# Kernel tuning notes

Hardware: AMD Instinct MI355X
Metric: run time of the kernel (lower is better)

The kernel has to match this reference:

```python
import jax, jax.numpy as jnp
import numpy as np

D_MODEL = 1024; D_STATE = 128; HEADDIM = 64; D_CONV = 4; CHUNK = 256
D_INNER = 2 * D_MODEL; NHEADS = D_INNER // HEADDIM
CONV_DIM = D_INNER + 2 * D_STATE
D_IN_PROJ = 2 * D_INNER + 2 * D_STATE + NHEADS
POOL_SIZE = 50; SUMMARY_DIM = 64; TAU1 = 0.5; TAU2 = 0.3
RET_HEAD_DIM = SUMMARY_DIM // 4  # CrossTokenRetrieval n_heads=4
SCORER_HID = int(D_MODEL * 0.25)
B_SZ = 2; T_LEN = 1024
EPS = 1e-5


def _rmsnorm(x, w):
    var = jnp.mean(jnp.square(x), axis=-1, keepdims=True)
    return x * jax.lax.rsqrt(var + EPS) * w


def _ssd(xd, dA, Bm, Cm):
    # Mamba2 SSD chunked scan. xd=(b,T,h,p)=x*dt, dA=(b,T,h)=dt*A, Bm/Cm=(b,T,n)
    b, T, h, p = xd.shape
    c = T // CHUNK; l = CHUNK
    xd = xd.reshape(b, c, l, h, p)
    dA = dA.reshape(b, c, l, h).transpose(0, 3, 1, 2)           # (b,h,c,l)
    Bm = Bm.reshape(b, c, l, -1); Cm = Cm.reshape(b, c, l, -1)  # (b,c,l,n)
    cs = jnp.cumsum(dA, axis=-1)                                # (b,h,c,l)
    mask = jnp.tril(jnp.ones((l, l), bool))
    seg = jnp.where(mask, cs[..., :, None] - cs[..., None, :], -jnp.inf)
    L = jnp.exp(seg)                                            # (b,h,c,l,s)
    y_diag = jnp.einsum('bcln,bcsn,bhcls,bcshp->bclhp', Cm, Bm, L, xd)
    decay_states = jnp.exp(cs[..., -1:] - cs)                   # (b,h,c,l)
    states = jnp.einsum('bcln,bhcl,bclhp->bchpn', Bm, decay_states, xd)
    chunk_sum = jnp.pad(cs[..., -1], ((0, 0), (0, 0), (1, 0)))  # (b,h,c+1)
    cs2 = jnp.cumsum(chunk_sum, axis=-1)
    maskc = jnp.tril(jnp.ones((c + 1, c + 1), bool))
    segc = jnp.where(maskc, cs2[..., :, None] - cs2[..., None, :], -jnp.inf)
    decay_chunk = jnp.exp(segc)                                 # (b,h,c+1,c+1)
    states = jnp.concatenate([jnp.zeros_like(states[:, :1]), states], axis=1)
    prev = jnp.einsum('bhzc,bchpn->bzhpn', decay_chunk, states)[:, :-1]
    y_off = jnp.einsum('bcln,bchpn,bhcl->bclhp', Cm, prev, jnp.exp(cs))
    return (y_diag + y_off).reshape(b, T, h, p)


def _forward(x, norm_w, in_proj_w, conv_w, conv_b, dt_bias, A_log, D, ssm_norm_w,
             out_proj_w, scorer_w1, scorer_w2, summ_w, q_w, k_w, v_w, gate_w):
    b, T, _ = x.shape
    residual = x
    xn = _rmsnorm(x, norm_w)
    # --- Mamba2 ---
    zxbcdt = xn @ in_proj_w                                     # (b,T,4384)
    z = zxbcdt[..., :D_INNER]
    xBC = zxbcdt[..., D_INNER:D_INNER + CONV_DIM]
    dt = jax.nn.softplus(zxbcdt[..., -NHEADS:] + dt_bias)       # (b,T,h)
    xpad = jnp.pad(xBC, ((0, 0), (D_CONV - 1, 0), (0, 0)))      # causal depthwise conv
    conv = conv_b + sum(xpad[:, k:k + T, :] * conv_w[:, k] for k in range(D_CONV))
    xBC = jax.nn.silu(conv)
    xs = xBC[..., :D_INNER].reshape(b, T, NHEADS, HEADDIM)
    Bm = xBC[..., D_INNER:D_INNER + D_STATE]
    Cm = xBC[..., D_INNER + D_STATE:]
    A = -jnp.exp(A_log)                                         # (h,)
    y = _ssd(xs * dt[..., None], dt * A, Bm, Cm)
    y = y + xs * D[None, None, :, None]
    y = y.reshape(b, T, D_INNER)
    y = _rmsnorm(y * jax.nn.silu(z), ssm_norm_w)                # gated RMSNorm
    y = y @ out_proj_w                                          # (b,T,d_model)
    # --- token importance scorer ---
    scores = jax.nn.sigmoid(jax.nn.relu(y @ scorer_w1) @ scorer_w2)[..., 0]  # (b,T)
    # --- memory pool update (layer_idx % freq == 0) ---
    summaries = (y @ summ_w).reshape(-1, SUMMARY_DIM)
    flat_scores = scores.reshape(-1)

    def step(carry, inp):
        pool, prios, count = carry
        s, sc = inp
        valid = sc > TAU1
        not_full = count < POOL_SIZE
        min_idx = jnp.argmin(prios)
        idx = jnp.where(not_full, count, min_idx)
        write = valid & (not_full | (sc > prios[min_idx]))
        pool = pool.at[idx].set(jnp.where(write, s, pool[idx]))
        prios = prios.at[idx].set(jnp.where(write, sc, prios[idx]))
        count = count + (valid & not_full).astype(jnp.int32)
        return (pool, prios, count), None

    init = (jnp.zeros((POOL_SIZE, SUMMARY_DIM), y.dtype),
            jnp.zeros((POOL_SIZE,), y.dtype), jnp.int32(0))
    (pool, prios, count), _ = jax.lax.scan(step, init, (summaries, flat_scores))
    # --- retrieval + gated fusion ---
    q = y @ q_w                                                 # (b,T,S)
    kk = pool @ k_w                                             # (P,S)
    vv = pool @ v_w                                             # (P,d_model)
    logits = jnp.einsum('bts,ps->btp', q, kk) / (RET_HEAD_DIM ** 0.5)
    valid_slot = jnp.arange(POOL_SIZE) < count
    logits = jnp.where(valid_slot, logits, -1e9)
    retrieved = jnp.einsum('btp,pd->btd', jax.nn.softmax(logits, axis=-1), vv)
    gate = jax.nn.sigmoid(jnp.concatenate([y, retrieved], axis=-1) @ gate_w)
    cond = (jnp.mean(scores) > TAU2) & (count > 0)
    y = jnp.where(cond, y + gate * retrieved, y)
    return residual + y


def setup_inputs() -> dict:
    key = jax.random.key(0)
    ks = jax.random.split(key, 16)
    w = lambda k, shape, s=0.02: jax.random.normal(k, shape, jnp.float32) * s
    dt = jax.random.uniform(ks[5], (NHEADS,), jnp.float32, 0.001, 0.1)
    return {
        'x': jax.random.normal(ks[0], (B_SZ, T_LEN, D_MODEL), jnp.float32),
        'norm_w': jnp.ones((D_MODEL,), jnp.float32),
        'in_proj_w': w(ks[1], (D_MODEL, D_IN_PROJ)),
        'conv_w': w(ks[2], (CONV_DIM, D_CONV), 0.1),
        'conv_b': jnp.zeros((CONV_DIM,), jnp.float32),
        'dt_bias': jnp.log(jnp.expm1(dt)),
        'A_log': jnp.log(jax.random.uniform(ks[6], (NHEADS,), jnp.float32, 1.0, 16.0)),
        'D': jnp.ones((NHEADS,), jnp.float32),
        'ssm_norm_w': jnp.ones((D_INNER,), jnp.float32),
        'out_proj_w': w(ks[7], (D_INNER, D_MODEL)),
        'scorer_w1': w(ks[8], (D_MODEL, SCORER_HID)),
        'scorer_w2': w(ks[9], (SCORER_HID, 1), 0.2),
        'summ_w': w(ks[10], (D_MODEL, SUMMARY_DIM)),
        'q_w': w(ks[11], (D_MODEL, SUMMARY_DIM)),
        'k_w': w(ks[12], (SUMMARY_DIM, SUMMARY_DIM)),
        'v_w': w(ks[13], (SUMMARY_DIM, D_MODEL)),
        'gate_w': w(ks[14], (2 * D_MODEL, D_MODEL)),
    }


def reference(x, norm_w, in_proj_w, conv_w, conv_b, dt_bias, A_log, D, ssm_norm_w,
              out_proj_w, scorer_w1, scorer_w2, summ_w, q_w, k_w, v_w, gate_w):
    return _forward(x, norm_w, in_proj_w, conv_w, conv_b, dt_bias, A_log, D, ssm_norm_w,
                    out_proj_w, scorer_w1, scorer_w2, summ_w, q_w, k_w, v_w, gate_w)
```

## Files before the change

### kernel.cpp

```cpp
#include <hip/hip_runtime.h>
#include <math.h>

#define NHEADS 32
#define D_INNER 2048
#define CONV_DIM 2304
#define D_IN_PROJ 4384
#define POOL_N 50
#define BT 2048

typedef __attribute__((ext_vector_type(8))) short short8;
typedef __attribute__((ext_vector_type(4))) float f32x4;

__device__ __forceinline__ float sigmoidf_(float x){ return 1.f/(1.f+expf(-x)); }
__device__ __forceinline__ ushort f2bf(float f){
  union{float f; unsigned u;} v; v.f=f;
  unsigned r = v.u + 0x7fffu + ((v.u>>16)&1u);
  return (ushort)(r>>16);
}
__device__ __forceinline__ void gload16(const void* g, void* l){
  __builtin_amdgcn_global_load_lds(
    (const __attribute__((address_space(1))) unsigned int*)g,
    (__attribute__((address_space(3))) unsigned int*)l, 16, 0, 0);
}

__global__ __launch_bounds__(256) void k_rmsnorm_x(const float* __restrict__ x, const float* __restrict__ w, ushort* __restrict__ xn){
  int r = blockIdx.x;
  const float* xr = x + (size_t)r*1024;
  float v[4]; float ss=0.f;
  for(int i=0;i<4;i++){ v[i]=xr[threadIdx.x+i*256]; ss+=v[i]*v[i]; }
  __shared__ float red[4];
  for(int off=32;off;off>>=1) ss += __shfl_down(ss,off,64);
  int wid=threadIdx.x>>6, lane=threadIdx.x&63;
  if(lane==0) red[wid]=ss;
  __syncthreads();
  float tot=red[0]+red[1]+red[2]+red[3];
  float rs=rsqrtf(tot*(1.f/1024.f)+1e-5f);
  for(int i=0;i<4;i++){ int c=threadIdx.x+i*256; xn[(size_t)r*1024+c]=f2bf(v[i]*rs*w[c]); }
}

__global__ __launch_bounds__(256) void k_transpose_cvt(const float* __restrict__ src, ushort* __restrict__ dst, int R, int C){
  __shared__ float tile[32][33];
  int c0 = blockIdx.x*32, r0 = blockIdx.y*32;
  int tx = threadIdx.x&31, ty = threadIdx.x>>5;
  for(int i=0;i<4;i++){ int r = r0+ty+i*8; tile[ty+i*8][tx] = src[(size_t)r*C + c0+tx]; }
  __syncthreads();
  for(int i=0;i<4;i++){ int c = c0+ty+i*8; dst[(size_t)c*R + r0+tx] = f2bf(tile[tx][ty+i*8]); }
}

__global__ __launch_bounds__(256) void gemm_bf16(const ushort* __restrict__ A, const ushort* __restrict__ Bt,
    float* __restrict__ C, ushort* __restrict__ Cb, int M, int N, int K, int act, int nbx){
  __shared__ __align__(16) ushort As[128*32];
  __shared__ __align__(16) ushort Bs[128*32];
  int wg = blockIdx.x, nwg = gridDim.x;
  if((nwg & 7)==0){ int cpx = nwg>>3; wg = (wg&7)*cpx + (wg>>3); }
  int bx = wg % nbx, by = wg / nbx;
  int n0 = bx*128, m0 = by*128;
  int tid = threadIdx.x;
  int lane = tid&63, w = tid>>6;
  int wr = (w>>1)*64, wc = (w&1)*64;
  f32x4 acc[4][4];
  for(int i=0;i<4;i++)for(int j=0;j<4;j++)acc[i][j]=(f32x4){0.f,0.f,0.f,0.f};
  int srow0 = w*32 + (lane>>2);
  int sbyte = (lane&3)*16;
  const char* AG0 = (const char*)(A + (size_t)(m0+srow0)*K) + sbyte;
  const char* AG1 = (const char*)(A + (size_t)(m0+srow0+16)*K) + sbyte;
  int brow0 = n0+srow0, brow1 = n0+srow0+16;
  bool bv0 = brow0 < N, bv1 = brow1 < N;
  const char* BG0 = (const char*)(Bt + (size_t)(bv0?brow0:0)*K) + sbyte;
  const char* BG1 = (const char*)(Bt + (size_t)(bv1?brow1:0)*K) + sbyte;
  char* Al0 = (char*)As + w*2048; char* Al1 = Al0 + 1024;
  char* Bl0 = (char*)Bs + w*2048; char* Bl1 = Bl0 + 1024;
  int fr = lane&15, fko = (lane>>4)*8;
  for(int k0=0;k0<K;k0+=32){
    gload16(AG0 + (size_t)k0*2, Al0);
    gload16(AG1 + (size_t)k0*2, Al1);
    if(bv0) gload16(BG0 + (size_t)k0*2, Bl0);
    if(bv1) gload16(BG1 + (size_t)k0*2, Bl1);
    __syncthreads();
    short8 af[4], bfr[4];
    for(int i=0;i<4;i++) af[i]  = *(const short8*)(As + (wr+i*16+fr)*32 + fko);
    for(int j=0;j<4;j++) bfr[j] = *(const short8*)(Bs + (wc+j*16+fr)*32 + fko);
    for(int i=0;i<4;i++)
      for(int j=0;j<4;j++)
        acc[i][j] = __builtin_amdgcn_mfma_f32_16x16x32_bf16(af[i], bfr[j], acc[i][j], 0,0,0);
    __syncthreads();
  }
  int rbase = m0 + wr + (lane>>4)*4;
  for(int i=0;i<4;i++){
    for(int j=0;j<4;j++){
      int col = n0 + wc + j*16 + fr;
      if(col < N){
        for(int r=0;r<4;r++){
          float v = acc[i][j][r];
          if(act) v = fmaxf(v,0.f);
          size_t idx = (size_t)(rbase + i*16 + r)*N + col;
          C[idx] = v;
          if(Cb) Cb[idx] = f2bf(v);
        }
      }
    }
  }
}

__global__ void k_dt(const float* __restrict__ zxb, const float* __restrict__ dt_bias, float* __restrict__ dtb){
  int o = blockIdx.x*256+threadIdx.x;
  int r = o>>5, h = o&31;
  float v = zxb[(size_t)r*D_IN_PROJ + 4352 + h] + dt_bias[h];
  dtb[o] = (v>20.f) ? v : log1pf(expf(v));
}

__global__ void k_conv4(const float* __restrict__ zxb, const float* __restrict__ cw, const float* __restrict__ cb, float* __restrict__ xbc){
  int o = blockIdx.x*256+threadIdx.x;
  if(o >= 2048*576) return;
  int ch4 = (o % 576)*4; int rt = o / 576;
  int b = rt>>10, t = rt&1023;
  float a[4];
  { float4 cbv = *(const float4*)(cb + ch4); a[0]=cbv.x; a[1]=cbv.y; a[2]=cbv.z; a[3]=cbv.w; }
  float cwa[4][4];
  for(int c2=0;c2<4;c2++){
    float4 v = *(const float4*)(cw + (ch4+c2)*4);
    cwa[c2][0]=v.x; cwa[c2][1]=v.y; cwa[c2][2]=v.z; cwa[c2][3]=v.w;
  }
  for(int k=0;k<4;k++){
    int tt = t-3+k;
    if(tt>=0){
      float4 v = *(const float4*)(zxb + (size_t)(b*1024+tt)*D_IN_PROJ + 2048 + ch4);
      a[0] += v.x*cwa[0][k]; a[1] += v.y*cwa[1][k];
      a[2] += v.z*cwa[2][k]; a[3] += v.w*cwa[3][k];
    }
  }
  float4 o4;
  o4.x = a[0]*sigmoidf_(a[0]); o4.y = a[1]*sigmoidf_(a[1]);
  o4.z = a[2]*sigmoidf_(a[2]); o4.w = a[3]*sigmoidf_(a[3]);
  *(float4*)(xbc + (size_t)rt*CONV_DIM + ch4) = o4;
}

__global__ __launch_bounds__(256) void k_gt(const float* __restrict__ xbc, float* __restrict__ Gt){
  int bc = blockIdx.x >> 8;
  int tile = blockIdx.x & 255;
  int l0 = (tile>>4)<<4, s0 = (tile&15)<<4;
  int b = bc>>2, c = bc&3;
  int row0 = b*1024 + c*256;
  __shared__ float Cs[16][130], Bs2[16][130];
  int tid = threadIdx.x;
  for(int i=0;i<8;i++){ int e=tid+i*256; int rr=e>>7, n=e&127;
    Cs[rr][n]  = xbc[(size_t)(row0+l0+rr)*CONV_DIM + 2176 + n];
    Bs2[rr][n] = xbc[(size_t)(row0+s0+rr)*CONV_DIM + 2048 + n];
  }
  __syncthreads();
  int tx = tid&15, ty = tid>>4;
  float acc=0.f;
  for(int n=0;n<128;n++) acc += Cs[tx][n]*Bs2[ty][n];
  Gt[(size_t)bc*65536 + (size_t)(s0+ty)*256 + (l0+tx)] = acc;
}

__global__ __launch_bounds__(512) void k_ssd1w(const float* __restrict__ xbc, const float* __restrict__ dtb,
    const float* __restrict__ A_log, const float* __restrict__ Gt,
    float* __restrict__ ybuf, float* __restrict__ states, float* __restrict__ csb, float* __restrict__ sdA){
  int blk = blockIdx.x;
  int bc = blk>>5, h = blk&31;
  int b = bc>>2, c = bc&3;
  int row0 = b*1024 + c*256;
  int tid = threadIdx.x;
  __shared__ float cs[256];
  __shared__ float dts[256];
  __shared__ float dec[256];
  __shared__ __align__(16) ushort xdT[64*256];
  __shared__ __align__(16) ushort Mw[4*64*32];
  __shared__ __align__(16) ushort Bw[4*32*256];
  float Ah = -expf(A_log[h]);
  if(tid < 256){
    float dtv = dtb[(size_t)(row0+tid)*32 + h];
    dts[tid] = dtv;
    cs[tid] = dtv*Ah;
  }
  __syncthreads();
  for(int o=1;o<256;o<<=1){
    float add = 0.f;
    if(tid<256 && tid>=o) add = cs[tid-o];
    __syncthreads();
    if(tid<256) cs[tid] += add;
    __syncthreads();
  }
  float cslast = cs[255];
  if(tid < 256){
    float csl = cs[tid];
    csb[blk*256+tid] = csl;
    dec[tid] = expf(cslast - csl);
    if(tid==0) sdA[blk] = cslast;
  }
  {
    int p = tid&63, g = tid>>6;
    for(int i=0;i<32;i++){
      int l = g + 8*i;
      float v = xbc[(size_t)(row0+l)*CONV_DIM + h*64 + p] * dts[l];
      int off = ((p<<9) + (l<<1)) ^ ((p&7)<<4);
      *(ushort*)((char*)xdT + off) = f2bf(v);
    }
  }
  __syncthreads();

  int w = tid>>6, lane = tid&63;
  int fr = lane&15, fq = lane>>4;
  const float* gt = Gt + (size_t)bc*65536;
  if(w < 4){
    int rowl = w*64 + lane;
    float csl_w = cs[rowl];
    f32x4 accY[4][4];
    for(int i=0;i<4;i++)for(int j=0;j<4;j++)accY[i][j]=(f32x4){0.f,0.f,0.f,0.f};
    int nk = 2*(w+1);
    for(int ks=0; ks<nk; ks++){
      int s0 = ks*32;
      float cs_s0 = cs[s0];
      float ev = expf(cs_s0 - cs[s0 + (lane&31)]);
      float el = expf(csl_w - cs_s0);
      for(int j=0;j<4;j++){
        short8 mp;
        for(int k=0;k<8;k++){
          int s2 = j*8+k;
          int s = s0 + s2;
          float gv = gt[(size_t)s*256 + rowl];
          float esv = __shfl(ev, s2, 64);
          float m = (s <= rowl) ? gv*el*esv : 0.f;
          mp[k] = (short)f2bf(m);
        }
        int off = (w<<12) + ((((lane)<<6) + (j<<4)) ^ ((lane&7)<<4));
        *(short8*)((char*)Mw + off) = mp;
      }
      asm volatile("s_waitcnt lgkmcnt(0)" ::: "memory");
      __builtin_amdgcn_sched_barrier(0);
      short8 af[4], bv4[4];
      for(int i=0;i<4;i++){
        int lp = i*16 + fr;
        int off = (w<<12) + (((lp<<6) + (fq<<4)) ^ ((lp&7)<<4));
        af[i] = *(const short8*)((char*)Mw + off);
      }
      for(int j=0;j<4;j++){
        int p = j*16 + fr;
        int off = ((p<<9) + ((s0 + fq*8)<<1)) ^ ((p&7)<<4);
        bv4[j] = *(const short8*)((char*)xdT + off);
      }
      for(int i=0;i<4;i++)
        for(int j=0;j<4;j++)
          accY[i][j] = __builtin_amdgcn_mfma_f32_16x16x32_bf16(af[i], bv4[j], accY[i][j], 0,0,0);
      asm volatile("" ::: "memory");
    }
    for(int i=0;i<4;i++){
      int l = 64*w + i*16 + fq*4;
      for(int j=0;j<4;j++){
        int p = j*16 + fr;
        for(int r=0;r<4;r++)
          ybuf[(size_t)(row0+l+r)*2048 + h*64 + p] = accY[i][j][r];
      }
    }
  } else {
    int sw = w-4, nbase = sw*32;
    {
      int nn = lane&31, half = lane>>5;
      for(int i=0;i<128;i++){
        int l = half + 2*i;
        float v = xbc[(size_t)(row0+l)*CONV_DIM + 2048 + nbase + nn] * dec[l];
        int off = (sw<<14) + (((nn<<9) + (l<<1)) ^ ((nn&7)<<4));
        *(ushort*)((char*)Bw + off) = f2bf(v);
      }
    }
    asm volatile("s_waitcnt lgkmcnt(0)" ::: "memory");
    __builtin_amdgcn_sched_barrier(0);
    f32x4 accS[4][2];
    for(int i=0;i<4;i++)for(int j=0;j<2;j++)accS[i][j]=(f32x4){0.f,0.f,0.f,0.f};
    for(int ks=0;ks<8;ks++){
      int l0 = ks*32;
      short8 aS[4], bS[2];
      for(int i=0;i<4;i++){
        int p = i*16 + fr;
        int off = ((p<<9) + ((l0+fq*8)<<1)) ^ ((p&7)<<4);
        aS[i] = *(const short8*)((char*)xdT + off);
      }
      for(int j=0;j<2;j++){
        int nn = j*16 + fr;
        int off = (sw<<14) + (((nn<<9) + ((l0+fq*8)<<1)) ^ ((nn&7)<<4));
        bS[j] = *(const short8*)((char*)Bw + off);
      }
      for(int i=0;i<4;i++)
        for(int j=0;j<2;j++)
          accS[i][j] = __builtin_amdgcn_mfma_f32_16x16x32_bf16(aS[i], bS[j], accS[i][j], 0,0,0);
    }
    for(int i=0;i<4;i++){
      int p = i*16 + fq*4;
      for(int j=0;j<2;j++){
        int n = nbase + j*16 + fr;
        for(int r=0;r<4;r++)
          states[(size_t)blk*8192 + (size_t)(p+r)*128 + n] = accS[i][j][r];
      }
    }
  }
}

__global__ __launch_bounds__(256) void k_ssd2(const float* __restrict__ states, const float* __restrict__ sdA, float* __restrict__ prevb){
  int idx = blockIdx.x*256 + threadIdx.x;
  int e = idx & 8191;
  int h = (idx >> 13) & 31;
  int b = idx >> 18;
  float run = 0.f;
  for(int c=0;c<4;c++){
    int sblk = (b*4+c)*32 + h;
    size_t base = (size_t)sblk*8192 + e;
    prevb[base] = run;
    run = (run + states[base]) * expf(sdA[sblk]);
  }
}

__global__ __launch_bounds__(256) void k_ssd3m(const float* __restrict__ xbc, const float* __restrict__ csb,
    const float* __restrict__ prevb, const float* __restrict__ Dp, float* __restrict__ ybuf){
  int blk = blockIdx.x; int bc = blk>>5, h = blk&31; int b=bc>>2, c=bc&3;
  int row0 = b*1024+c*256;
  int tid = threadIdx.x;
  __shared__ __align__(16) ushort Cs[256*128];
  __shared__ __align__(16) ushort Ps[64*128];
  __shared__ float cse[256];
  for(int i=0;i<128;i++){
    int id = tid + i*256;
    int n = id & 127, l = id >> 7;
    float v = xbc[(size_t)(row0+l)*CONV_DIM + 2176 + n];
    int off = ((l<<8) + (n<<1)) ^ ((l&7)<<4);
    *(ushort*)((char*)Cs + off) = f2bf(v);
  }
  for(int i=0;i<32;i++){
    int id = tid + i*256;
    int n = id & 127, p = id >> 7;
    float v = prevb[(size_t)blk*8192 + id];
    int off = ((p<<8) + (n<<1)) ^ ((p&7)<<4);
    *(ushort*)((char*)Ps + off) = f2bf(v);
  }
  cse[tid] = expf(csb[blk*256+tid]);
  __syncthreads();
  int w=tid>>6, lane=tid&63, fr=lane&15, fq=lane>>4;
  f32x4 acc[4][4];
  for(int i=0;i<4;i++)for(int j=0;j<4;j++)acc[i][j]=(f32x4){0.f,0.f,0.f,0.f};
  for(int ks=0;ks<4;ks++){
    int n0 = ks*32;
    short8 af[4], bf_[4];
    for(int i=0;i<4;i++){
      int l = w*64 + i*16 + fr;
      int off = ((l<<8) + ((n0+fq*8)<<1)) ^ ((l&7)<<4);
      af[i] = *(const short8*)((char*)Cs + off);
    }
    for(int j=0;j<4;j++){
      int p = j*16 + fr;
      int off = ((p<<8) + ((n0+fq*8)<<1)) ^ ((p&7)<<4);
      bf_[j] = *(const short8*)((char*)Ps + off);
    }
    for(int i=0;i<4;i++)
      for(int j=0;j<4;j++)
        acc[i][j] = __builtin_amdgcn_mfma_f32_16x16x32_bf16(af[i], bf_[j], acc[i][j], 0,0,0);
  }
  float Dh = Dp[h];
  for(int i=0;i<4;i++){
    int lbase = 64*w + i*16 + fq*4;
    for(int r=0;r<4;r++){
      int l = lbase + r;
      float e = cse[l];
      size_t rowoff = (size_t)(row0+l)*CONV_DIM + h*64;
      size_t yb = (size_t)(row0+l)*2048 + h*64;
      for(int j=0;j<4;j++){
        int p = j*16 + fr;
        float xs = xbc[rowoff + p];
        ybuf[yb+p] += e*acc[i][j][r] + xs*Dh;
      }
    }
  }
}

__global__ __launch_bounds__(256) void k_gate_norm(const float* __restrict__ y, const float* __restrict__ zxb,
    const float* __restrict__ w, ushort* __restrict__ yb16){
  int r = blockIdx.x;
  const float* zr = zxb + (size_t)r*D_IN_PROJ;
  const float* yr = y + (size_t)r*2048;
  float v[8]; float ss=0.f;
  for(int i=0;i<8;i++){ int c=threadIdx.x+i*256; float z=zr[c]; float g=yr[c]*(z*sigmoidf_(z)); v[i]=g; ss+=g*g; }
  __shared__ float red[4];
  for(int off=32;off;off>>=1) ss += __shfl_down(ss,off,64);
  int wid=threadIdx.x>>6, lane=threadIdx.x&63;
  if(lane==0) red[wid]=ss;
  __syncthreads();
  float tot=red[0]+red[1]+red[2]+red[3];
  float rs=rsqrtf(tot*(1.f/2048.f)+1e-5f);
  for(int i=0;i<8;i++){ int c=threadIdx.x+i*256; yb16[(size_t)r*2048+c]=f2bf(v[i]*rs*w[c]); }
}

__global__ void k_scorer2(const float* __restrict__ h1, const float* __restrict__ w2, float* __restrict__ scores){
  int r = blockIdx.x; int lane = threadIdx.x;
  float s=0.f;
  for(int k=0;k<4;k++){ int c=lane+k*64; s += h1[(size_t)r*256+c]*w2[c]; }
  for(int off=32;off;off>>=1) s += __shfl_down(s,off,64);
  if(lane==0) scores[r]=sigmoidf_(s);
}

__global__ void k_pool(const float* __restrict__ scores,
                       int* __restrict__ countws, int* __restrict__ winners, float* __restrict__ condf){
  __shared__ float scs[BT];
  int lane = threadIdx.x;
  float own[32];
  float ssum = 0.f; int vcnt = 0;
  #pragma unroll
  for(int i=0;i<32;i++){
    float s0 = scores[i*64 + lane];
    own[i] = s0; scs[i*64+lane] = s0;
    ssum += s0; vcnt += (s0 > 0.5f) ? 1 : 0;
  }
  float ts = ssum; int tv = vcnt;
  for(int off=32;off;off>>=1){ ts += __shfl_xor(ts,off,64); tv += __shfl_xor(tv,off,64); }
  int count = tv < POOL_N ? tv : POOL_N;
  bool fallback = false;
  if(tv <= POOL_N){
    int base = 0;
    #pragma unroll
    for(int i=0;i<32;i++){
      bool sel = own[i] > 0.5f;
      unsigned long long mask = __ballot(sel);
      int pre = __popcll(mask & ((1ull<<lane)-1ull));
      if(sel) winners[base + pre] = i*64 + lane;
      base += __popcll(mask);
    }
    for(int r=base+lane; r<POOL_N; r+=64) winners[r] = -1;
  } else {
    unsigned lo = 0u, hi = 0x3F800000u;
    while(hi - lo > 1u){
      unsigned mid = (lo + hi) >> 1;
      float midf = __uint_as_float(mid);
      int cnt = 0;
      #pragma unroll
      for(int i=0;i<32;i++) cnt += (own[i] >= midf) ? 1 : 0;
      for(int off=32;off;off>>=1) cnt += __shfl_xor(cnt,off,64);
      if(cnt >= POOL_N) lo = mid; else hi = mid;
    }
    float v50 = __uint_as_float(lo);
    int cl = 0;
    #pragma unroll
    for(int i=0;i<32;i++) cl += (own[i] >= v50) ? 1 : 0;
    for(int off=32;off;off>>=1) cl += __shfl_xor(cl,off,64);
    if(cl == POOL_N){
      int base = 0;
      #pragma unroll
      for(int i=0;i<32;i++){
        bool sel = own[i] >= v50;
        unsigned long long mask = __ballot(sel);
        int pre = __popcll(mask & ((1ull<<lane)-1ull));
        if(sel) winners[base + pre] = i*64 + lane;
        base += __popcll(mask);
      }
    } else fallback = true;
  }
  if(fallback){
    float prio = 0.f; int winner = -1; int cnt2 = 0;
    float curmin = 0.f; int curargmin = 0;
    for(int b0=0;b0<BT;b0+=64){
      float ow = scs[b0+lane];
      unsigned long long mask = (cnt2 < POOL_N) ? __ballot(ow > 0.5f) : __ballot(ow > curmin);
      while(mask){
        int j = __ffsll(mask) - 1;
        mask &= mask - 1ull;
        float sc = __shfl(ow, j, 64);
        if(cnt2 < POOL_N){
          if(lane == cnt2){ prio = sc; winner = b0+j; }
          cnt2++;
          if(cnt2 == POOL_N){
            float v = (lane < POOL_N)? prio : INFINITY; int idx = lane;
            for(int off=32;off;off>>=1){
              float ov = __shfl_xor(v,off,64); int oi = __shfl_xor(idx,off,64);
              if(ov < v || (ov==v && oi<idx)){ v=ov; idx=oi; }
            }
            curmin = v; curargmin = idx;
          }
        } else if(sc > curmin){
          if(lane == curargmin){ prio = sc; winner = b0+j; }
          float v = (lane < POOL_N)? prio : INFINITY; int idx = lane;
          for(int off=32;off;off>>=1){
            float ov = __shfl_xor(v,off,64); int oi = __shfl_xor(idx,off,64);
            if(ov < v || (ov==v && oi<idx)){ v=ov; idx=oi; }
          }
          curmin = v; curargmin = idx;
        }
      }
    }
    if(lane < POOL_N) winners[lane] = winner;
  }
  if(lane==0){
    countws[0] = count;
    float mean = ts*(1.f/2048.f);
    condf[0] = (mean>0.3f && count>0)? 1.f : 0.f;
  }
}

__global__ void k_poolg(const float* __restrict__ sq, const int* __restrict__ winners, float* __restrict__ poolb){
  int p = blockIdx.x; int lane = threadIdx.x;
  int wi = winners[p];
  poolb[p*64+lane] = (wi>=0)? sq[(size_t)wi*128+lane] : 0.f;
}

__global__ void k_kk(const float* __restrict__ pool, const float* __restrict__ k_w, float* __restrict__ kkT){
  int o = blockIdx.x*256+threadIdx.x;
  if(o >= 64*POOL_N) return;
  int j = o/POOL_N, p = o%POOL_N;
  float s=0.f;
  for(int k=0;k<64;k++) s += pool[p*64+k]*k_w[k*64+j];
  kkT[j*64+p]=s;
}

__global__ void k_vvT(const float* __restrict__ pool, const float* __restrict__ v_w, ushort* __restrict__ vvT){
  int o = blockIdx.x*256+threadIdx.x;
  if(o >= 1024*64) return;
  int d = o>>6, p = o&63;
  float s=0.f;
  if(p < POOL_N)
    for(int k=0;k<64;k++) s += pool[p*64+k]*v_w[(size_t)k*1024+d];
  vvT[o] = f2bf(s);
}

__global__ __launch_bounds__(256) void k_probs(const float* __restrict__ sq, const float* __restrict__ kkT,
    const int* __restrict__ counti, ushort* __restrict__ Pb){
  __shared__ float qs[4][64];
  int tid = threadIdx.x;
  int w = tid>>6, lane = tid&63;
  int r = blockIdx.x*4 + w;
  qs[w][lane] = sq[(size_t)r*128 + 64 + lane];
  __syncthreads();
  int count = counti[0];
  float logit = -1e9f;
  if(lane < POOL_N && lane < count){
    float s=0.f;
    for(int k=0;k<64;k++) s += qs[w][k]*kkT[k*64+lane];
    logit = s*0.25f;
  }
  float m = logit;
  for(int off=32;off;off>>=1) m = fmaxf(m, __shfl_xor(m,off,64));
  float e = expf(logit-m);
  float sum = e;
  for(int off=32;off;off>>=1) sum += __shfl_xor(sum,off,64);
  Pb[(size_t)r*64 + lane] = f2bf(e/sum);
}

__global__ __launch_bounds__(256) void k_pv(const ushort* __restrict__ Pb, const ushort* __restrict__ vvT,
    float* __restrict__ retr){
  __shared__ __align__(16) ushort As[128*64];
  __shared__ __align__(16) ushort Bs[128*64];
  int m0 = (blockIdx.x >> 3)*128, n0 = (blockIdx.x & 7)*128;
  int tid = threadIdx.x;
  int row = tid>>1, half = tid&1;
  {
    const uint4* sa = (const uint4*)(Pb  + (size_t)(m0+row)*64 + half*32);
    const uint4* sb = (const uint4*)(vvT + (size_t)(n0+row)*64 + half*32);
    for(int ch=0;ch<4;ch++){
      int boff = (row<<7) + (half<<6) + (ch<<4);
      int so = boff ^ ((row&7)<<4);
      *(uint4*)((char*)As + so) = sa[ch];
      *(uint4*)((char*)Bs + so) = sb[ch];
    }
  }
  __syncthreads();
  int w=tid>>6, lane=tid&63, fr=lane&15, fq=lane>>4;
  int wr=(w>>1)*64, wc=(w&1)*64;
  f32x4 acc[4][4];
  for(int i=0;i<4;i++)for(int j=0;j<4;j++)acc[i][j]=(f32x4){0.f,0.f,0.f,0.f};
  for(int k0=0;k0<64;k0+=32){
    short8 af[4], bf_[4];
    for(int i=0;i<4;i++){
      int r = wr+i*16+fr;
      int boff = ((r<<7) + ((k0+fq*8)<<1)) ^ ((r&7)<<4);
      af[i] = *(const short8*)((char*)As + boff);
    }
    for(int j=0;j<4;j++){
      int r = wc+j*16+fr;
      int boff = ((r<<7) + ((k0+fq*8)<<1)) ^ ((r&7)<<4);
      bf_[j] = *(const short8*)((char*)Bs + boff);
    }
    for(int i=0;i<4;i++)
      for(int j=0;j<4;j++)
        acc[i][j] = __builtin_amdgcn_mfma_f32_16x16x32_bf16(af[i], bf_[j], acc[i][j], 0,0,0);
  }
  int rbase = m0 + wr + fq*4;
  for(int i=0;i<4;i++){
    for(int j=0;j<4;j++){
      int col = n0 + wc + j*16 + fr;
      for(int r=0;r<4;r++)
        retr[(size_t)(rbase + i*16 + r)*1024 + col] = acc[i][j][r];
    }
  }
}

__global__ void k_concat(const float* __restrict__ yout, const float* __restrict__ retr, ushort* __restrict__ cc){
  int o = blockIdx.x*256+threadIdx.x;
  int r = o>>11, c2 = o&2047;
  cc[o] = f2bf((c2<1024)? yout[(size_t)r*1024+c2] : retr[(size_t)r*1024+(c2-1024)]);
}

__global__ void k_final(const float* __restrict__ x, const float* __restrict__ yout, const float* __restrict__ g,
   const float* __restrict__ retr, const float* __restrict__ condf, float* __restrict__ out){
  int o = blockIdx.x*256+threadIdx.x;
  float gv = sigmoidf_(g[o]);
  out[o] = x[o] + yout[o] + condf[0]*gv*retr[o];
}

static inline void gemmb(hipStream_t s, const ushort*A,const ushort*Bt,float*C,ushort*Cb,int M,int N,int K,int act){
  int nbx = (N+127)/128;
  int nwg = nbx * (M/128);
  hipLaunchKernelGGL(gemm_bf16,dim3(nwg),dim3(256),0,s,A,Bt,C,Cb,M,N,K,act,nbx);
}

extern "C" void kernel_launch(void* const* d_in, const int* in_sizes, int n_in,
                              void* d_out, int out_size, void* d_ws, size_t ws_size,
                              hipStream_t stream) {
  const float* x        = (const float*)d_in[0];
  const float* norm_w   = (const float*)d_in[1];
  const float* in_proj_w= (const float*)d_in[2];
  const float* conv_w   = (const float*)d_in[3];
  const float* conv_b   = (const float*)d_in[4];
  const float* dt_bias  = (const float*)d_in[5];
  const float* A_log    = (const float*)d_in[6];
  const float* Dp       = (const float*)d_in[7];
  const float* ssm_norm_w=(const float*)d_in[8];
  const float* out_proj_w=(const float*)d_in[9];
  const float* scorer_w1= (const float*)d_in[10];
  const float* scorer_w2= (const float*)d_in[11];
  const float* summ_w   = (const float*)d_in[12];
  const float* q_w      = (const float*)d_in[13];
  const float* k_w      = (const float*)d_in[14];
  const float* v_w      = (const float*)d_in[15];
  const float* gate_w   = (const float*)d_in[16];
  float* out = (float*)d_out;

  unsigned char* base = (unsigned char*)d_ws;
  size_t off = 0;
  auto FB = [&](size_t bytes)->void*{ void* p = base+off; off = (off+bytes+255)&~(size_t)255; return p; };
  float* zxb   = (float*)FB((size_t)2048*D_IN_PROJ*4);
  float* dtb   = (float*)FB((size_t)2048*32*4);
  float* xbc   = (float*)FB((size_t)2048*CONV_DIM*4);
  float* csb   = (float*)FB((size_t)256*256*4);
  float* sdA   = (float*)FB(1024);
  float* states= (float*)FB((size_t)256*8192*4);
  float* prevb = (float*)FB((size_t)256*8192*4);
  float* ybuf  = (float*)FB((size_t)2048*2048*4);
  float* yout  = (float*)FB((size_t)2048*1024*4);
  float* scores= (float*)FB(2048*4);
  float* summ  = (float*)FB((size_t)2048*64*4);
  float* qb    = (float*)FB((size_t)2048*64*4);
  float* poolb = (float*)FB(POOL_N*64*4);
  float* prios = (float*)FB(256);
  float* miscf = (float*)FB(256);
  int*   counti= (int*)FB(256);
  int*   winners=(int*)FB(256);
  unsigned char* RX = (unsigned char*)FB((size_t)4194304);
  unsigned char* W1 = (unsigned char*)FB((size_t)8978432);

  ushort* xnb   = (ushort*)RX;
  ushort* sqT   = (ushort*)RX;
  ushort* summT = (ushort*)RX;
  ushort* qT    = (ushort*)(RX + 131072);
  float*  h1    = (float*) (RX + 262144);
  float*  kkT   = (float*) (RX + 2359296);
  ushort* vvT   = (ushort*)(RX + 2375680);
  ushort* Pb    = (ushort*)(RX + 2506752);
  ushort* inT   = (ushort*)W1;
  ushort* outT  = (ushort*)W1;
  ushort* gateT = (ushort*)(W1 + 4194304);
  ushort* sc1T  = (ushort*)(W1 + 8388608);
  float*  Gt    = yout;
  ushort* ybf   = (ushort*)prevb;
  float*  gbuf  = prevb;
  float*  retr  = states;
  ushort* ccb   = (ushort*)ybuf;
  ushort* youtb = (ushort*)((unsigned char*)ybuf + 8388608);
  float*  sq    = summ;
  (void)qb; (void)prios;

  hipLaunchKernelGGL(k_transpose_cvt, dim3(137,32), dim3(256), 0, stream, in_proj_w, inT, 1024, 4384);
  k_rmsnorm_x<<<2048,256,0,stream>>>(x, norm_w, xnb);
  gemmb(stream, xnb, inT, zxb, nullptr, 2048, D_IN_PROJ, 1024, 0);
  hipLaunchKernelGGL(k_transpose_cvt, dim3(32,64), dim3(256), 0, stream, out_proj_w, outT, 2048, 1024);
  hipLaunchKernelGGL(k_transpose_cvt, dim3(32,64), dim3(256), 0, stream, gate_w, gateT, 2048, 1024);
  hipLaunchKernelGGL(k_transpose_cvt, dim3(8,32), dim3(256), 0, stream, scorer_w1, sc1T, 1024, 256);
  hipLaunchKernelGGL(k_transpose_cvt, dim3(2,32), dim3(256), 0, stream, summ_w, summT, 1024, 64);
  hipLaunchKernelGGL(k_transpose_cvt, dim3(2,32), dim3(256), 0, stream, q_w, qT, 1024, 64);
  k_dt<<<256,256,0,stream>>>(zxb, dt_bias, dtb);
  k_conv4<<<4608,256,0,stream>>>(zxb, conv_w, conv_b, xbc);
  k_gt<<<2048,256,0,stream>>>(xbc, Gt);
  k_ssd1w<<<256,512,0,stream>>>(xbc, dtb, A_log, Gt, ybuf, states, csb, sdA);
  k_ssd2<<<2048,256,0,stream>>>(states, sdA, prevb);
  k_ssd3m<<<256,256,0,stream>>>(xbc, csb, prevb, Dp, ybuf);
  k_gate_norm<<<2048,256,0,stream>>>(ybuf, zxb, ssm_norm_w, ybf);
  gemmb(stream, ybf, outT, yout, youtb, 2048, 1024, 2048, 0);
  gemmb(stream, youtb, sc1T, h1, nullptr, 2048, 256, 1024, 1);
  k_scorer2<<<2048,64,0,stream>>>(h1, scorer_w2, scores);
  gemmb(stream, youtb, sqT, sq, nullptr, 2048, 128, 1024, 0);
  k_pool<<<1,64,0,stream>>>(scores, counti, winners, miscf);
  k_poolg<<<POOL_N,64,0,stream>>>(sq, winners, poolb);
  k_kk<<<(64*POOL_N+255)/256,256,0,stream>>>(poolb, k_w, kkT);
  k_vvT<<<256,256,0,stream>>>(poolb, v_w, vvT);
  k_probs<<<512,256,0,stream>>>(sq, kkT, counti, Pb);
  k_pv<<<128,256,0,stream>>>(Pb, vvT, retr);
  k_concat<<<16384,256,0,stream>>>(yout, retr, ccb);
  gemmb(stream, ccb, gateT, gbuf, nullptr, 2048, 1024, 2048, 0);
  k_final<<<8192,256,0,stream>>>(x, yout, gbuf, retr, miscf, out);
  (void)in_sizes; (void)n_in; (void)out_size; (void)ws_size;
}
```

Before: 332.4 us.

## Double-buffer GEMM LDS tiles with BK=64 and XOR-swizzled layout

Rewrites the bf16 GEMM main loop to use two LDS buffers with a K-tile of 64, prefetching the next tile via global_load_lds while MFMAs run on the current one. Manual vmcnt waits and barriers replace the two __syncthreads per step. An XOR swizzle on the 16-byte column index is meant to avoid LDS bank conflicts on the fragment reads. LDS use grows fourfold, which may lower occupancy, and it assumes K is a multiple of 64 and that the hand-placed waitcnt ordering is correct.

```diff
diff --git a/kernel.cpp b/kernel.cpp
--- a/kernel.cpp
+++ b/kernel.cpp
@@ -49,8 +49,8 @@
 
 __global__ __launch_bounds__(256) void gemm_bf16(const ushort* __restrict__ A, const ushort* __restrict__ Bt,
     float* __restrict__ C, ushort* __restrict__ Cb, int M, int N, int K, int act, int nbx){
-  __shared__ __align__(16) ushort As[128*32];
-  __shared__ __align__(16) ushort Bs[128*32];
+  __shared__ __align__(16) ushort As[2][128*64];
+  __shared__ __align__(16) ushort Bs[2][128*64];
   int wg = blockIdx.x, nwg = gridDim.x;
   if((nwg & 7)==0){ int cpx = nwg>>3; wg = (wg&7)*cpx + (wg>>3); }
   int bx = wg % nbx, by = wg / nbx;
@@ -60,32 +60,66 @@
   int wr = (w>>1)*64, wc = (w&1)*64;
   f32x4 acc[4][4];
   for(int i=0;i<4;i++)for(int j=0;j<4;j++)acc[i][j]=(f32x4){0.f,0.f,0.f,0.f};
-  int srow0 = w*32 + (lane>>2);
-  int sbyte = (lane&3)*16;
-  const char* AG0 = (const char*)(A + (size_t)(m0+srow0)*K) + sbyte;
-  const char* AG1 = (const char*)(A + (size_t)(m0+srow0+16)*K) + sbyte;
-  int brow0 = n0+srow0, brow1 = n0+srow0+16;
-  bool bv0 = brow0 < N, bv1 = brow1 < N;
-  const char* BG0 = (const char*)(Bt + (size_t)(bv0?brow0:0)*K) + sbyte;
-  const char* BG1 = (const char*)(Bt + (size_t)(bv1?brow1:0)*K) + sbyte;
-  char* Al0 = (char*)As + w*2048; char* Al1 = Al0 + 1024;
-  char* Bl0 = (char*)Bs + w*2048; char* Bl1 = Bl0 + 1024;
-  int fr = lane&15, fko = (lane>>4)*8;
-  for(int k0=0;k0<K;k0+=32){
-    gload16(AG0 + (size_t)k0*2, Al0);
-    gload16(AG1 + (size_t)k0*2, Al1);
-    if(bv0) gload16(BG0 + (size_t)k0*2, Bl0);
-    if(bv1) gload16(BG1 + (size_t)k0*2, Bl1);
-    __syncthreads();
-    short8 af[4], bfr[4];
-    for(int i=0;i<4;i++) af[i]  = *(const short8*)(As + (wr+i*16+fr)*32 + fko);
-    for(int j=0;j<4;j++) bfr[j] = *(const short8*)(Bs + (wc+j*16+fr)*32 + fko);
-    for(int i=0;i<4;i++)
-      for(int j=0;j<4;j++)
-        acc[i][j] = __builtin_amdgcn_mfma_f32_16x16x32_bf16(af[i], bfr[j], acc[i][j], 0,0,0);
-    __syncthreads();
-  }
-  int rbase = m0 + wr + (lane>>4)*4;
+  int col16s = (tid&7) ^ ((tid>>3)&7);
+  int r0t = tid>>3;
+  const char* AG[4]; const char* BG[4];
+  #pragma unroll
+  for(int c=0;c<4;c++){
+    int r = r0t + c*32;
+    AG[c] = (const char*)(A + (size_t)(m0+r)*K + col16s*8);
+    int br = n0 + r;
+    BG[c] = (const char*)(Bt + (size_t)((br<N)?br:0)*K + col16s*8);
+  }
+  int nk = K >> 6;
+  int fr = lane&15, fq = lane>>4;
+  {
+    #pragma unroll
+    for(int c=0;c<4;c++){
+      gload16(AG[c], (char*)As[0] + (c*256 + w*64)*16);
+      gload16(BG[c], (char*)Bs[0] + (c*256 + w*64)*16);
+    }
+  }
+  for(int ks=0; ks<nk; ks++){
+    int cur = ks&1;
+    if(ks+1 < nk){
+      size_t kb = (size_t)(ks+1)*128;
+      #pragma unroll
+      for(int c=0;c<4;c++){
+        gload16(AG[c]+kb, (char*)As[cur^1] + (c*256 + w*64)*16);
+        gload16(BG[c]+kb, (char*)Bs[cur^1] + (c*256 + w*64)*16);
+      }
+      asm volatile("s_waitcnt vmcnt(8)" ::: "memory");
+    } else {
+      asm volatile("s_waitcnt vmcnt(0)" ::: "memory");
+    }
+    __builtin_amdgcn_s_barrier();
+    __builtin_amdgcn_sched_barrier(0);
+    #pragma unroll
+    for(int kk=0;kk<2;kk++){
+      short8 af[4], bfr[4];
+      #pragma unroll
+      for(int i=0;i<4;i++){
+        int rl = wr+i*16+fr;
+        int off = ((rl<<7) + (kk<<6) + (fq<<4)) ^ ((rl&7)<<4);
+        af[i] = *(const short8*)((char*)As[cur] + off);
+      }
+      #pragma unroll
+      for(int j=0;j<4;j++){
+        int rl = wc+j*16+fr;
+        int off = ((rl<<7) + (kk<<6) + (fq<<4)) ^ ((rl&7)<<4);
+        bfr[j] = *(const short8*)((char*)Bs[cur] + off);
+      }
+      #pragma unroll
+      for(int i=0;i<4;i++)
+        #pragma unroll
+        for(int j=0;j<4;j++)
+          acc[i][j] = __builtin_amdgcn_mfma_f32_16x16x32_bf16(af[i], bfr[j], acc[i][j], 0,0,0);
+    }
+    asm volatile("s_waitcnt lgkmcnt(0)" ::: "memory");
+    __builtin_amdgcn_sched_barrier(0);
+    __builtin_amdgcn_s_barrier();
+  }
+  int rbase = m0 + wr + fq*4;
   for(int i=0;i<4;i++){
     for(int j=0;j<4;j++){
       int col = n0 + wc + j*16 + fr;
```

Measured after the change: 323.5 us. 2.7% less time.
